# Kernel optimization log

Measured on AMD Instinct MI355X. Metric: run time of the kernel, lower is better.

## Reference

```python
import jax, jax.numpy as jnp
import numpy as np

B, T, C, H = 2, 2048, 1024, 16
HD = C // H          # head_dim = 64
RD = HD // 2         # rotary half-dim = 32


def _rope_tables(T, rd, base=10000.0):
    inv_freq = 1.0 / (base ** (np.arange(rd, dtype=np.float32) / rd))
    t = np.arange(T, dtype=np.float32)
    ang = np.outer(t, inv_freq)  # [T, rd]
    cos = np.cos(ang)[None, :, None, :]  # [1,T,1,rd]
    sin = np.sin(ang)[None, :, None, :]
    return jnp.asarray(cos), jnp.asarray(sin)


def setup_inputs() -> dict:
    key = jax.random.key(0)
    k1, k2, k3 = jax.random.split(key, 3)
    cos, sin = _rope_tables(T, RD)
    return {
        "x": jax.random.normal(k1, (B, T, C), dtype=jnp.float32),
        "cos": cos,
        "sin": sin,
        "W_qkv": jax.random.normal(k2, (C, C), dtype=jnp.float32) / np.sqrt(C),
        "W_proj": jax.random.normal(k3, (C, C), dtype=jnp.float32) / np.sqrt(C),
        "window_left": 512,
    }


def _apply_rotary(x, cos, sin):
    # x: [B,T,H,HD]
    x1, x2 = x[..., :RD], x[..., RD:]
    y1 = x1 * cos + x2 * sin
    y2 = -x1 * sin + x2 * cos
    return jnp.concatenate([y1, y2], axis=-1)


def _rms_norm(x):
    eps = jnp.finfo(x.dtype).eps
    ms = jnp.mean(jnp.square(x), axis=-1, keepdims=True)
    return x * jax.lax.rsqrt(ms + eps)


def reference(x, cos, sin, W_qkv, W_proj, window_left):
    Bx, Tx, Cx = x.shape
    scale = HD ** -0.5
    # tied QKV projection (single matmul)
    w = jnp.einsum("btc,cd->btd", x, W_qkv).reshape(Bx, Tx, H, HD)
    w = _apply_rotary(w, cos, sin)
    w = _rms_norm(w)                      # [B,T,H,HD]
    wq = jnp.transpose(w, (0, 2, 1, 3))    # [B,H,T,HD]
    dots = jnp.einsum("bhqd,bhkd->bhqk", wq, wq) * scale  # [B,H,T,T]
    # causal + sliding-window mask: allow 0 <= (q - k) <= window_left
    i = jnp.arange(Tx)[:, None]
    j = jnp.arange(Tx)[None, :]
    dist = i - j
    allowed = (dist >= 0) & ((window_left <= 0) | (dist <= window_left))
    dots = jnp.where(allowed, dots, -jnp.inf)
    attn = jax.nn.softmax(dots, axis=-1)
    out = jnp.einsum("bhqk,bhkd->bhqd", attn, wq)
    out = jnp.transpose(out, (0, 2, 1, 3)).reshape(Bx, Tx, Cx)
    return jnp.einsum("btc,cd->btd", out, W_proj)
```

## Files before the change

kernel.cpp:

```cpp
#include <hip/hip_runtime.h>
#include <hip/hip_bf16.h>

typedef __bf16 bf16_t;
typedef __bf16 bf16x4 __attribute__((ext_vector_type(4)));
typedef __bf16 bf16x8 __attribute__((ext_vector_type(8)));
typedef float f32x4 __attribute__((ext_vector_type(4)));

#define B_ 2
#define T_ 2048
#define C_ 1024
#define H_ 16
#define HD_ 64
#define RD_ 32
#define M_ (B_ * T_)

__global__ __launch_bounds__(256) void k_prep(const float* __restrict__ x,
                                              bf16_t* __restrict__ xb,
                                              const float* __restrict__ Wq,
                                              bf16_t* __restrict__ wqt,
                                              const float* __restrict__ Wp,
                                              bf16_t* __restrict__ wpt) {
    const int bid = blockIdx.x;
    if (bid < 4096) {
        int i = bid * 256 + threadIdx.x;
        float4 v = reinterpret_cast<const float4*>(x)[i];
        bf16x4 o;
        o[0] = (bf16_t)v.x; o[1] = (bf16_t)v.y; o[2] = (bf16_t)v.z; o[3] = (bf16_t)v.w;
        reinterpret_cast<bf16x4*>(xb)[i] = o;
    } else {
        __shared__ float tile[32][33];
        int b2 = bid - 4096;
        const float* W = (b2 < 1024) ? Wq : Wp;
        bf16_t* Wt = (b2 < 1024) ? wqt : wpt;
        b2 &= 1023;
        const int n0 = (b2 & 31) * 32, k0 = (b2 >> 5) * 32;
        const int tx = threadIdx.x & 31, ty = threadIdx.x >> 5;
        for (int i = ty; i < 32; i += 8)
            tile[i][tx] = W[(size_t)(k0 + i) * C_ + n0 + tx];
        __syncthreads();
        for (int i = ty; i < 32; i += 8)
            Wt[(size_t)(n0 + i) * C_ + k0 + tx] = (bf16_t)tile[tx][i];
    }
}

template <bool FUSED>
__global__ __launch_bounds__(256) void k_gemm(const bf16_t* __restrict__ A,
                                              const bf16_t* __restrict__ Bt,
                                              float* __restrict__ C,
                                              const float* __restrict__ ct,
                                              const float* __restrict__ st,
                                              bf16_t* __restrict__ q,
                                              bf16_t* __restrict__ qT,
                                              int M, int N, int K) {
    constexpr int SMEM_BYTES = FUSED ? 52224 : 49152;
    __shared__ __align__(16) char smem[SMEM_BYTES];
    bf16_t* As = (bf16_t*)smem;
    bf16_t* Bs = (bf16_t*)(smem + 32768);
    const int tid = threadIdx.x;
    const int lane = tid & 63, w = tid >> 6;
    const int wr = w >> 1, wc = w & 1;
    const int g = lane >> 4, li = lane & 15;
    const int bid = blockIdx.x;
    const int work = (bid & 7) * 64 + (bid >> 3);
    const int bx = work & 15;
    const int by = work >> 4;
    const size_t rowA0 = (size_t)by * 128;
    const size_t colB0 = (size_t)bx * 64;
    const bf16_t* Ab = A + rowA0 * K;
    const bf16_t* Bb = Bt + colB0 * K;
    f32x4 acc[4][2] = {};

    const int lr = lane >> 3;
    const int swc = ((lane & 7) ^ lr) * 8;

    auto stage = [&](int buf, int k0) {
        bf16_t* Ad = As + buf * 8192 + (w * 8) * 64;
        bf16_t* Bd = Bs + buf * 4096 + (w * 8) * 64;
#pragma unroll
        for (int a = 0; a < 4; ++a) {
            const bf16_t* src = Ab + (size_t)(a * 32 + w * 8 + lr) * K + k0 + swc;
            __builtin_amdgcn_global_load_lds(
                (const __attribute__((address_space(1))) void*)src,
                (__attribute__((address_space(3))) void*)(Ad + a * 32 * 64), 16, 0, 0);
        }
#pragma unroll
        for (int bq = 0; bq < 2; ++bq) {
            const bf16_t* src = Bb + (size_t)(bq * 32 + w * 8 + lr) * K + k0 + swc;
            __builtin_amdgcn_global_load_lds(
                (const __attribute__((address_space(1))) void*)src,
                (__attribute__((address_space(3))) void*)(Bd + bq * 32 * 64), 16, 0, 0);
        }
    };

    stage(0, 0);
    __syncthreads();
    int cur = 0;
    const int NT = K >> 6;
    for (int kt = 0; kt < NT; ++kt) {
        if (kt < NT - 1) stage(cur ^ 1, (kt + 1) << 6);
        bf16x8 af[4][2], bfr[2][2];
#pragma unroll
        for (int i = 0; i < 4; ++i) {
            const int row = wr * 64 + i * 16 + li;
#pragma unroll
            for (int kk = 0; kk < 2; ++kk)
                af[i][kk] = *(const bf16x8*)(As + cur * 8192 + row * 64 +
                                             (((kk * 4 + g) ^ (li & 7)) * 8));
        }
#pragma unroll
        for (int j = 0; j < 2; ++j) {
            const int row = wc * 32 + j * 16 + li;
#pragma unroll
            for (int kk = 0; kk < 2; ++kk)
                bfr[j][kk] = *(const bf16x8*)(Bs + cur * 4096 + row * 64 +
                                              (((kk * 4 + g) ^ (li & 7)) * 8));
        }
#pragma unroll
        for (int i = 0; i < 4; ++i)
#pragma unroll
            for (int j = 0; j < 2; ++j)
#pragma unroll
                for (int kk = 0; kk < 2; ++kk)
                    acc[i][j] = __builtin_amdgcn_mfma_f32_16x16x32_bf16(
                        af[i][kk], bfr[j][kk], acc[i][j], 0, 0, 0);
        __syncthreads();
        cur ^= 1;
    }

    if constexpr (!FUSED) {
#pragma unroll
        for (int i = 0; i < 4; ++i)
#pragma unroll
            for (int j = 0; j < 2; ++j)
#pragma unroll
                for (int r = 0; r < 4; ++r) {
                    size_t row = rowA0 + wr * 64 + i * 16 + g * 4 + r;
                    size_t col = colB0 + wc * 32 + j * 16 + li;
                    C[row * N + col] = acc[i][j][r];
                }
    } else {
        float* ot = (float*)smem;
        bf16_t* qs = (bf16_t*)(smem + 34816);
#pragma unroll
        for (int i = 0; i < 4; ++i)
#pragma unroll
            for (int j = 0; j < 2; ++j)
#pragma unroll
                for (int r = 0; r < 4; ++r)
                    ot[(wr * 64 + i * 16 + g * 4 + r) * 68 + wc * 32 + j * 16 + li] =
                        acc[i][j][r];
        __syncthreads();
        {
            const int row = tid >> 1, half = tid & 1;
            const int gr = (int)rowA0 + row;
            const int bb = gr >> 11, t = gr & 2047;
            const float* own = ot + row * 68 + half * 32;
            const float* par = ot + row * 68 + (half ^ 1) * 32;
            const float* cp = ct + (size_t)t * RD_;
            const float* sp = st + (size_t)t * RD_;
            float y[32];
            float sq = 0.f;
#pragma unroll
            for (int c4 = 0; c4 < 8; ++c4) {
                float4 xo = ((const float4*)own)[c4];
                float4 xp = ((const float4*)par)[c4];
                float4 cc = ((const float4*)cp)[c4];
                float4 ss = ((const float4*)sp)[c4];
                float* yy = y + c4 * 4;
                if (half == 0) {
                    yy[0] = xo.x * cc.x + xp.x * ss.x;
                    yy[1] = xo.y * cc.y + xp.y * ss.y;
                    yy[2] = xo.z * cc.z + xp.z * ss.z;
                    yy[3] = xo.w * cc.w + xp.w * ss.w;
                } else {
                    yy[0] = xo.x * cc.x - xp.x * ss.x;
                    yy[1] = xo.y * cc.y - xp.y * ss.y;
                    yy[2] = xo.z * cc.z - xp.z * ss.z;
                    yy[3] = xo.w * cc.w - xp.w * ss.w;
                }
                sq += yy[0] * yy[0] + yy[1] * yy[1] + yy[2] * yy[2] + yy[3] * yy[3];
            }
            sq += __shfl_xor(sq, 1);
            const float rn = rsqrtf(sq * (1.0f / 64.0f) + 1.1920929e-7f);
            bf16_t yb[32];
#pragma unroll
            for (int e = 0; e < 32; ++e) yb[e] = (bf16_t)(y[e] * rn);
            bf16_t* qrow = q + (((size_t)bb * H_ + bx) * T_ + t) * 64 + half * 32;
#pragma unroll
            for (int c8 = 0; c8 < 4; ++c8)
                ((bf16x8*)qrow)[c8] = *(const bf16x8*)(yb + c8 * 8);
#pragma unroll
            for (int e = 0; e < 32; ++e)
                qs[(half * 32 + e) * 136 + row] = yb[e];
        }
        __syncthreads();
        {
            const int d = tid >> 2, tq = tid & 3;
            const int bb = (int)(rowA0 >> 11);
            const int t0 = (int)(rowA0 & 2047);
            const bf16_t* srcq = qs + d * 136 + tq * 32;
            bf16_t* dst = qT + (((size_t)bb * H_ + bx) * 64 + d) * T_ + t0 + tq * 32;
#pragma unroll
            for (int c8 = 0; c8 < 4; ++c8)
                ((bf16x8*)dst)[c8] = ((const bf16x8*)srcq)[c8];
        }
    }
}

__global__ __launch_bounds__(256, 2) void k_attn(const bf16_t* __restrict__ q,
                                                 const bf16_t* __restrict__ qT,
                                                 bf16_t* __restrict__ aout,
                                                 const int* __restrict__ wlp) {
    __shared__ bf16_t Ks[2][64][64];
    __shared__ bf16_t Vs[2][64][64];
    __shared__ bf16_t pb[4][16][40];
    const int tid = threadIdx.x;
    const int lane = tid & 63, w = tid >> 6;
    const int g = lane >> 4, li = lane & 15;
    const int bid = blockIdx.x;
    const int work = (bid & 7) * 128 + (bid >> 3);
    const int tb = work & 31;
    const int h = (work >> 5) & 15;
    const int b = work >> 9;
    const int Q0 = tb * 64;
    const bf16_t* base  = q  + ((size_t)(b * H_ + h) * T_) * 64;
    const bf16_t* baseT = qT + ((size_t)(b * H_ + h) * 64) * T_;
    const int wl = wlp[0];
    const int wle = (wl <= 0 || wl > T_) ? T_ : wl;
    const int qw = Q0 + w * 16;
    const int qg = qw + li;

    const int r0 = tid >> 3, c0 = tid & 7;
    const int r1 = r0 + 32;
    const int sw0 = (c0 ^ (r0 & 7)) * 8;
    const int sw1 = (c0 ^ (r1 & 7)) * 8;

    bf16x8 aq[2];
    aq[0] = *reinterpret_cast<const bf16x8*>(base + (size_t)(qw + li) * 64 + g * 8);
    aq[1] = *reinterpret_cast<const bf16x8*>(base + (size_t)(qw + li) * 64 + 32 + g * 8);

    f32x4 o[4] = {};
    float m = -1e30f, l = 0.f;

    const int kb0 = (Q0 > wle) ? ((Q0 - wle) >> 6) : 0;
    const int kb1 = Q0 >> 6;

    {
        const int J0 = kb0 << 6;
        bf16x8 ka = *reinterpret_cast<const bf16x8*>(base + (size_t)(J0 + r0) * 64 + c0 * 8);
        bf16x8 kb_ = *reinterpret_cast<const bf16x8*>(base + (size_t)(J0 + r1) * 64 + c0 * 8);
        bf16x8 va = *reinterpret_cast<const bf16x8*>(baseT + (size_t)r0 * T_ + J0 + c0 * 8);
        bf16x8 vb = *reinterpret_cast<const bf16x8*>(baseT + (size_t)r1 * T_ + J0 + c0 * 8);
        *reinterpret_cast<bf16x8*>(&Ks[0][r0][sw0]) = ka;
        *reinterpret_cast<bf16x8*>(&Ks[0][r1][sw1]) = kb_;
        *reinterpret_cast<bf16x8*>(&Vs[0][r0][sw0]) = va;
        *reinterpret_cast<bf16x8*>(&Vs[0][r1][sw1]) = vb;
    }
    __syncthreads();

    int cur = 0;
    for (int kb = kb0; kb <= kb1; ++kb) {
        const int J0 = kb << 6;
        const bool pre = (kb < kb1);
        bf16x8 ka, kb_, va, vb;
        if (pre) {
            const int Jn = (kb + 1) << 6;
            ka  = *reinterpret_cast<const bf16x8*>(base + (size_t)(Jn + r0) * 64 + c0 * 8);
            kb_ = *reinterpret_cast<const bf16x8*>(base + (size_t)(Jn + r1) * 64 + c0 * 8);
            va  = *reinterpret_cast<const bf16x8*>(baseT + (size_t)r0 * T_ + Jn + c0 * 8);
            vb  = *reinterpret_cast<const bf16x8*>(baseT + (size_t)r1 * T_ + Jn + c0 * 8);
        }
        f32x4 s4[4] = {};
#pragma unroll
        for (int ks = 0; ks < 2; ++ks)
#pragma unroll
            for (int nb = 0; nb < 4; ++nb) {
                const int jl = nb * 16 + li;
                bf16x8 kf = *reinterpret_cast<const bf16x8*>(
                    &Ks[cur][jl][((ks * 4 + g) ^ (jl & 7)) * 8]);
                s4[nb] = __builtin_amdgcn_mfma_f32_16x16x32_bf16(kf, aq[ks], s4[nb], 0, 0, 0);
            }
        float sv[4][4];
        float mn = m;
#pragma unroll
        for (int nb = 0; nb < 4; ++nb)
#pragma unroll
            for (int r = 0; r < 4; ++r) {
                const int j = J0 + nb * 16 + g * 4 + r;
                const int dist = qg - j;
                float x = s4[nb][r] * 0.125f;
                sv[nb][r] = (dist >= 0 && dist <= wle) ? x : -__builtin_inff();
                mn = fmaxf(mn, sv[nb][r]);
            }
        mn = fmaxf(mn, __shfl_xor(mn, 16));
        mn = fmaxf(mn, __shfl_xor(mn, 32));
        const float al = __expf(m - mn);
        m = mn;
        float la = 0.f;
#pragma unroll
        for (int nb = 0; nb < 4; ++nb)
#pragma unroll
            for (int r = 0; r < 4; ++r) {
                float pv = __expf(sv[nb][r] - m);
                sv[nb][r] = pv;
                la += pv;
            }
        la += __shfl_xor(la, 16);
        la += __shfl_xor(la, 32);
        l = l * al + la;
        float alq[4];
#pragma unroll
        for (int r = 0; r < 4; ++r) alq[r] = __shfl(al, g * 4 + r);
#pragma unroll
        for (int dnb = 0; dnb < 4; ++dnb)
#pragma unroll
            for (int r = 0; r < 4; ++r) o[dnb][r] *= alq[r];
#pragma unroll
        for (int ks = 0; ks < 2; ++ks) {
#pragma unroll
            for (int nb2 = 0; nb2 < 2; ++nb2) {
                const int nb = ks * 2 + nb2;
                bf16x4 pk;
                pk[0] = (bf16_t)sv[nb][0]; pk[1] = (bf16_t)sv[nb][1];
                pk[2] = (bf16_t)sv[nb][2]; pk[3] = (bf16_t)sv[nb][3];
                *reinterpret_cast<bf16x4*>(&pb[w][li][nb2 * 16 + g * 4]) = pk;
            }
            bf16x8 pa = *reinterpret_cast<const bf16x8*>(&pb[w][li][g * 8]);
#pragma unroll
            for (int dnb = 0; dnb < 4; ++dnb) {
                const int dl = dnb * 16 + li;
                bf16x8 vf = *reinterpret_cast<const bf16x8*>(
                    &Vs[cur][dl][((ks * 4 + g) ^ (dl & 7)) * 8]);
                o[dnb] = __builtin_amdgcn_mfma_f32_16x16x32_bf16(pa, vf, o[dnb], 0, 0, 0);
            }
        }
        if (pre) {
            *reinterpret_cast<bf16x8*>(&Ks[cur ^ 1][r0][sw0]) = ka;
            *reinterpret_cast<bf16x8*>(&Ks[cur ^ 1][r1][sw1]) = kb_;
            *reinterpret_cast<bf16x8*>(&Vs[cur ^ 1][r0][sw0]) = va;
            *reinterpret_cast<bf16x8*>(&Vs[cur ^ 1][r1][sw1]) = vb;
        }
        __syncthreads();
        cur ^= 1;
    }

    const float rli = 1.0f / l;
    float rlq[4];
#pragma unroll
    for (int r = 0; r < 4; ++r) rlq[r] = __shfl(rli, g * 4 + r);
#pragma unroll
    for (int dnb = 0; dnb < 4; ++dnb)
#pragma unroll
        for (int r = 0; r < 4; ++r) {
            size_t t = (size_t)qw + g * 4 + r;
            aout[((size_t)b * T_ + t) * C_ + h * 64 + dnb * 16 + li] =
                (bf16_t)(o[dnb][r] * rlq[r]);
        }
}

extern "C" void kernel_launch(void* const* d_in, const int* in_sizes, int n_in,
                              void* d_out, int out_size, void* d_ws, size_t ws_size,
                              hipStream_t stream) {
    const float* x     = (const float*)d_in[0];
    const float* ct    = (const float*)d_in[1];
    const float* st    = (const float*)d_in[2];
    const float* Wqkv  = (const float*)d_in[3];
    const float* Wproj = (const float*)d_in[4];
    const int*   wl    = (const int*)d_in[5];
    float* out = (float*)d_out;
    char* ws = (char*)d_ws;

    bf16_t* xb    = (bf16_t*)(ws);
    bf16_t* wqkvt = (bf16_t*)(ws + (8ull << 20));
    bf16_t* wprot = (bf16_t*)(ws + (10ull << 20));
    bf16_t* q     = (bf16_t*)(ws + (12ull << 20));
    bf16_t* qT    = (bf16_t*)(ws + (20ull << 20));
    bf16_t* ao    = (bf16_t*)(ws + (28ull << 20));

    k_prep<<<dim3(6144), dim3(256), 0, stream>>>(x, xb, Wqkv, wqkvt, Wproj, wprot);
    k_gemm<true><<<dim3(512), dim3(256), 0, stream>>>(xb, wqkvt, nullptr, ct, st,
                                                      q, qT, M_, C_, C_);
    k_attn<<<dim3(1024), dim3(256), 0, stream>>>(q, qT, ao, wl);
    k_gemm<false><<<dim3(512), dim3(256), 0, stream>>>(ao, wprot, out, nullptr, nullptr,
                                                       nullptr, nullptr, M_, C_, C_);
}
```

Baseline: 71.68 us.

## Stage K/V tiles via direct global-to-LDS loads, exp2 softmax, setprio around MFMA

The attention kernel now loads K and V tiles straight from global memory into LDS with global_load_lds, replacing the register round-trip and separate LDS stores. The XOR swizzle moves to the global source address so the existing swizzled LDS read pattern still holds. Softmax switches to exp2 with log2(e) folded into the scale. The MFMA sections are wrapped in s_setprio, and the occupancy hint is raised to 4 blocks per CU. The intent is to cut VGPR pressure and load/store instruction overhead, at the risk of wait-count and synchronisation subtleties with asynchronous LDS writes.

New measurement: 76.21 us. 1.06x slower.

```diff
diff --git a/kernel.cpp b/kernel.cpp
--- a/kernel.cpp
+++ b/kernel.cpp
@@ -207,7 +207,7 @@
     }
 }
 
-__global__ __launch_bounds__(256, 2) void k_attn(const bf16_t* __restrict__ q,
+__global__ __launch_bounds__(256, 4) void k_attn(const bf16_t* __restrict__ q,
                                                  const bf16_t* __restrict__ qT,
                                                  bf16_t* __restrict__ aout,
                                                  const int* __restrict__ wlp) {
@@ -230,10 +230,8 @@
     const int qw = Q0 + w * 16;
     const int qg = qw + li;
 
-    const int r0 = tid >> 3, c0 = tid & 7;
-    const int r1 = r0 + 32;
-    const int sw0 = (c0 ^ (r0 & 7)) * 8;
-    const int sw1 = (c0 ^ (r1 & 7)) * 8;
+    const int srow = w * 8 + (lane >> 3);
+    const int swz = ((lane & 7) ^ (lane >> 3)) * 8;
 
     bf16x8 aq[2];
     aq[0] = *reinterpret_cast<const bf16x8*>(base + (size_t)(qw + li) * 64 + g * 8);
@@ -241,36 +239,39 @@
 
     f32x4 o[4] = {};
     float m = -1e30f, l = 0.f;
+    const float SC = 0.125f * 1.44269504089f;
 
     const int kb0 = (Q0 > wle) ? ((Q0 - wle) >> 6) : 0;
     const int kb1 = Q0 >> 6;
 
-    {
-        const int J0 = kb0 << 6;
-        bf16x8 ka = *reinterpret_cast<const bf16x8*>(base + (size_t)(J0 + r0) * 64 + c0 * 8);
-        bf16x8 kb_ = *reinterpret_cast<const bf16x8*>(base + (size_t)(J0 + r1) * 64 + c0 * 8);
-        bf16x8 va = *reinterpret_cast<const bf16x8*>(baseT + (size_t)r0 * T_ + J0 + c0 * 8);
-        bf16x8 vb = *reinterpret_cast<const bf16x8*>(baseT + (size_t)r1 * T_ + J0 + c0 * 8);
-        *reinterpret_cast<bf16x8*>(&Ks[0][r0][sw0]) = ka;
-        *reinterpret_cast<bf16x8*>(&Ks[0][r1][sw1]) = kb_;
-        *reinterpret_cast<bf16x8*>(&Vs[0][r0][sw0]) = va;
-        *reinterpret_cast<bf16x8*>(&Vs[0][r1][sw1]) = vb;
-    }
+    auto stageKV = [&](int buf, int J) {
+        const bf16_t* ks0 = base + (size_t)(J + srow) * 64 + swz;
+        const bf16_t* ks1 = base + (size_t)(J + srow + 32) * 64 + swz;
+        const bf16_t* vs0 = baseT + (size_t)srow * T_ + J + swz;
+        const bf16_t* vs1 = baseT + (size_t)(srow + 32) * T_ + J + swz;
+        __builtin_amdgcn_global_load_lds(
+            (const __attribute__((address_space(1))) void*)ks0,
+            (__attribute__((address_space(3))) void*)(&Ks[buf][w * 8][0]), 16, 0, 0);
+        __builtin_amdgcn_global_load_lds(
+            (const __attribute__((address_space(1))) void*)ks1,
+            (__attribute__((address_space(3))) void*)(&Ks[buf][w * 8 + 32][0]), 16, 0, 0);
+        __builtin_amdgcn_global_load_lds(
+            (const __attribute__((address_space(1))) void*)vs0,
+            (__attribute__((address_space(3))) void*)(&Vs[buf][w * 8][0]), 16, 0, 0);
+        __builtin_amdgcn_global_load_lds(
+            (const __attribute__((address_space(1))) void*)vs1,
+            (__attribute__((address_space(3))) void*)(&Vs[buf][w * 8 + 32][0]), 16, 0, 0);
+    };
+
+    stageKV(0, kb0 << 6);
     __syncthreads();
 
     int cur = 0;
     for (int kb = kb0; kb <= kb1; ++kb) {
         const int J0 = kb << 6;
-        const bool pre = (kb < kb1);
-        bf16x8 ka, kb_, va, vb;
-        if (pre) {
-            const int Jn = (kb + 1) << 6;
-            ka  = *reinterpret_cast<const bf16x8*>(base + (size_t)(Jn + r0) * 64 + c0 * 8);
-            kb_ = *reinterpret_cast<const bf16x8*>(base + (size_t)(Jn + r1) * 64 + c0 * 8);
-            va  = *reinterpret_cast<const bf16x8*>(baseT + (size_t)r0 * T_ + Jn + c0 * 8);
-            vb  = *reinterpret_cast<const bf16x8*>(baseT + (size_t)r1 * T_ + Jn + c0 * 8);
-        }
+        if (kb < kb1) stageKV(cur ^ 1, J0 + 64);
         f32x4 s4[4] = {};
+        __builtin_amdgcn_s_setprio(1);
 #pragma unroll
         for (int ks = 0; ks < 2; ++ks)
 #pragma unroll
@@ -280,6 +281,7 @@
                     &Ks[cur][jl][((ks * 4 + g) ^ (jl & 7)) * 8]);
                 s4[nb] = __builtin_amdgcn_mfma_f32_16x16x32_bf16(kf, aq[ks], s4[nb], 0, 0, 0);
             }
+        __builtin_amdgcn_s_setprio(0);
         float sv[4][4];
         float mn = m;
 #pragma unroll
@@ -288,20 +290,20 @@
             for (int r = 0; r < 4; ++r) {
                 const int j = J0 + nb * 16 + g * 4 + r;
                 const int dist = qg - j;
-                float x = s4[nb][r] * 0.125f;
+                float x = s4[nb][r] * SC;
                 sv[nb][r] = (dist >= 0 && dist <= wle) ? x : -__builtin_inff();
                 mn = fmaxf(mn, sv[nb][r]);
             }
         mn = fmaxf(mn, __shfl_xor(mn, 16));
         mn = fmaxf(mn, __shfl_xor(mn, 32));
-        const float al = __expf(m - mn);
+        const float al = exp2f(m - mn);
         m = mn;
         float la = 0.f;
 #pragma unroll
         for (int nb = 0; nb < 4; ++nb)
 #pragma unroll
             for (int r = 0; r < 4; ++r) {
-                float pv = __expf(sv[nb][r] - m);
+                float pv = exp2f(sv[nb][r] - m);
                 sv[nb][r] = pv;
                 la += pv;
             }
@@ -326,6 +328,7 @@
                 *reinterpret_cast<bf16x4*>(&pb[w][li][nb2 * 16 + g * 4]) = pk;
             }
             bf16x8 pa = *reinterpret_cast<const bf16x8*>(&pb[w][li][g * 8]);
+            __builtin_amdgcn_s_setprio(1);
 #pragma unroll
             for (int dnb = 0; dnb < 4; ++dnb) {
                 const int dl = dnb * 16 + li;
@@ -333,12 +336,7 @@
                     &Vs[cur][dl][((ks * 4 + g) ^ (dl & 7)) * 8]);
                 o[dnb] = __builtin_amdgcn_mfma_f32_16x16x32_bf16(pa, vf, o[dnb], 0, 0, 0);
             }
-        }
-        if (pre) {
-            *reinterpret_cast<bf16x8*>(&Ks[cur ^ 1][r0][sw0]) = ka;
-            *reinterpret_cast<bf16x8*>(&Ks[cur ^ 1][r1][sw1]) = kb_;
-            *reinterpret_cast<bf16x8*>(&Vs[cur ^ 1][r0][sw0]) = va;
-            *reinterpret_cast<bf16x8*>(&Vs[cur ^ 1][r1][sw1]) = vb;
+            __builtin_amdgcn_s_setprio(0);
         }
         __syncthreads();
         cur ^= 1;
```
